# Optimization experiments

Hardware: AMD Instinct MI355X
Metric: run time of the kernel (lower is better)

Reference implementation:

```python
import jax, jax.numpy as jnp
import numpy as np

EMBED = 1024
HEADS = 16
HEAD_DIM = EMBED // HEADS

def setup_inputs() -> dict:
    key = jax.random.key(0)
    k1, k2, k3, k4, k5 = jax.random.split(key, 5)
    scale = 1.0 / np.sqrt(EMBED)
    return {
        "x": jax.random.normal(k1, (4, 2048, EMBED), dtype=jnp.float32),
        "qkv_w": jax.random.uniform(k2, (3 * EMBED, EMBED), minval=-scale, maxval=scale, dtype=jnp.float32),
        "qkv_b": jax.random.uniform(k3, (3 * EMBED,), minval=-scale, maxval=scale, dtype=jnp.float32),
        "out_w": jax.random.uniform(k4, (EMBED, EMBED), minval=-scale, maxval=scale, dtype=jnp.float32),
        "out_b": jax.random.uniform(k5, (EMBED,), minval=-scale, maxval=scale, dtype=jnp.float32),
    }

def reference(x, qkv_w, qkv_b, out_w, out_b):
    b, n, _ = x.shape
    # torch Linear: x @ W.T + b
    qkv = (jnp.einsum('bne,fe->bnf', x, qkv_w) + qkv_b).reshape(b, n, 3, HEADS, HEAD_DIM)
    q, k, v = qkv[:, :, 0], qkv[:, :, 1], qkv[:, :, 2]
    scores = jnp.einsum('bnhd,bmhd->bhnm', q, k) / jnp.sqrt(jnp.float32(HEAD_DIM))
    attn = jax.nn.softmax(scores, axis=-1)  # dropout p=0.0 -> identity
    out = jnp.einsum('bhnm,bmhd->bnhd', attn, v).reshape(b, n, EMBED)
    return jnp.einsum('bne,fe->bnf', out, out_w) + out_b
```

## Files before the change

kernel.cpp:

```cpp
#include <hip/hip_runtime.h>
#include <hip/hip_bf16.h>

typedef __bf16 bf16;
typedef __attribute__((ext_vector_type(8))) __bf16 bf16x8;
typedef __attribute__((ext_vector_type(4))) __bf16 bf16x4;
typedef __attribute__((ext_vector_type(4))) float f32x4;

#define EMBED 1024
#define HEADS 16
#define HD 64
#define NB 4
#define SEQ 2048
#define TOK (NB * SEQ)
#define F3 (3 * EMBED)

#define QSCALE 0.18033688011112042f
#define CEXP 16.0f

__device__ __forceinline__ float exp2_hw(float x) {
  float r;
  asm("v_exp_f32 %0, %1" : "=v"(r) : "v"(x));
  return r;
}

__device__ __forceinline__ void gload_lds16(const void* g, void* l) {
  __builtin_amdgcn_global_load_lds(
      (const __attribute__((address_space(1))) unsigned int*)(unsigned long long)g,
      (__attribute__((address_space(3))) unsigned int*)(unsigned int)(unsigned long long)l,
      16, 0, 0);
}

__global__ void cvt_bf16_kernel(const float* __restrict__ in, bf16* __restrict__ out, int n4) {
  int i = blockIdx.x * blockDim.x + threadIdx.x;
  if (i < n4) {
    float4 v = ((const float4*)in)[i];
    bf16x4 o;
    o[0] = (bf16)v.x; o[1] = (bf16)v.y; o[2] = (bf16)v.z; o[3] = (bf16)v.w;
    ((bf16x4*)out)[i] = o;
  }
}

template <int MODE, typename OUT_T>
__global__ __launch_bounds__(256) void gemm_bt(const bf16* __restrict__ A,
                                               const bf16* __restrict__ Bw,
                                               const float* __restrict__ bias,
                                               OUT_T* __restrict__ C,
                                               bf16* __restrict__ VT,
                                               int K, int Ncols) {
  __shared__ __align__(16) bf16 As[2][128 * 32];
  __shared__ __align__(16) bf16 Bs[2][128 * 32];

  const int tid = threadIdx.x;
  const int lane = tid & 63;
  const int w = tid >> 6;
  const int wr = w >> 1, wc = w & 1;
  const int lr = lane & 15, lg = lane >> 4;

  const int r0 = tid >> 2;
  const int csw = ((tid & 3) ^ ((tid >> 3) & 3)) * 8;
  const bf16* Ag = A + (size_t)blockIdx.x * 128 * K + (size_t)r0 * K + csw;
  const bf16* Bg = Bw + (size_t)blockIdx.y * 128 * K + (size_t)r0 * K + csw;

  f32x4 acc[4][4] = {};
  const int co = (lg ^ ((lr >> 1) & 3)) * 8;
  const int ntiles = K >> 5;

#define GSTAGE(buf)                                      \
  do {                                                   \
    gload_lds16(Ag, &As[buf][tid * 8]);                  \
    gload_lds16(Ag + 64 * K, &As[buf][(tid + 256) * 8]); \
    gload_lds16(Bg, &Bs[buf][tid * 8]);                  \
    gload_lds16(Bg + 64 * K, &Bs[buf][(tid + 256) * 8]); \
    Ag += 32; Bg += 32;                                  \
  } while (0)

  GSTAGE(0);
  __syncthreads();

  for (int t = 0; t < ntiles; ++t) {
    const int cur = t & 1;
    if (t + 1 < ntiles) GSTAGE(cur ^ 1);

    bf16x8 af[4], bfr[4];
#pragma unroll
    for (int mi = 0; mi < 4; ++mi)
      af[mi] = *(const bf16x8*)&As[cur][(wr * 64 + mi * 16 + lr) * 32 + co];
#pragma unroll
    for (int ni = 0; ni < 4; ++ni)
      bfr[ni] = *(const bf16x8*)&Bs[cur][(wc * 64 + ni * 16 + lr) * 32 + co];

#pragma unroll
    for (int mi = 0; mi < 4; ++mi)
#pragma unroll
      for (int ni = 0; ni < 4; ++ni)
        acc[mi][ni] = __builtin_amdgcn_mfma_f32_16x16x32_bf16(af[mi], bfr[ni], acc[mi][ni], 0, 0, 0);

    __syncthreads();
  }
#undef GSTAGE

  const int rowb = blockIdx.x * 128 + wr * 64;
  const int colb = blockIdx.y * 128 + wc * 64;

  if (MODE == 1 && blockIdx.y >= 16) {
#pragma unroll
    for (int ni = 0; ni < 4; ++ni) {
      int col = colb + ni * 16 + lr;
      int fc = col - 2 * EMBED;
      int hh = fc >> 6, d = fc & 63;
      float bv = bias[col];
#pragma unroll
      for (int mi = 0; mi < 4; ++mi) {
        int row = rowb + mi * 16 + lg * 4;
        int bb = row >> 11, nn = row & 2047;
        bf16x4 pk;
#pragma unroll
        for (int j = 0; j < 4; ++j) pk[j] = (bf16)(acc[mi][ni][j] + bv);
        *(bf16x4*)&VT[((size_t)((bb * HEADS + hh) * HD + d)) * SEQ + nn] = pk;
      }
    }
  } else {
    const float scale = (MODE == 1 && blockIdx.y < 8) ? QSCALE : 1.0f;
#pragma unroll
    for (int ni = 0; ni < 4; ++ni) {
      int col = colb + ni * 16 + lr;
      float bv = bias[col];
#pragma unroll
      for (int mi = 0; mi < 4; ++mi) {
#pragma unroll
        for (int j = 0; j < 4; ++j) {
          int row = rowb + mi * 16 + lg * 4 + j;
          C[(size_t)row * Ncols + col] = (OUT_T)((acc[mi][ni][j] + bv) * scale);
        }
      }
    }
  }
}

__global__ __launch_bounds__(256) void attn_fwd(const bf16* __restrict__ QK,
                                                const bf16* __restrict__ VT,
                                                bf16* __restrict__ O) {
  __shared__ __align__(16) bf16 Kb[2][64 * 64];
  __shared__ __align__(16) bf16 Vb[2][64 * 64];
  __shared__ __align__(16) bf16 Pl[4][32 * 76];

  const int qb = blockIdx.x, h = blockIdx.y, b = blockIdx.z;
  const int tid = threadIdx.x, lane = tid & 63, w = tid >> 6;
  const int lr = lane & 15, lg = lane >> 4;

  bf16x8 qf[2][2];
#pragma unroll
  for (int mi = 0; mi < 2; ++mi) {
    const bf16* qp = QK + (size_t)(b * SEQ + qb * 128 + w * 32 + mi * 16 + lr) * 2048 + h * HD + lg * 8;
    qf[mi][0] = *(const bf16x8*)qp;
    qf[mi][1] = *(const bf16x8*)(qp + 32);
  }

  const int rk = tid >> 3;
  const int cc = ((tid & 7) ^ (rk & 7)) * 8;
  const bf16* kp = QK + (size_t)(b * SEQ + rk) * 2048 + EMBED + h * HD + cc;
  const bf16* vp = VT + ((size_t)((b * HEADS + h) * HD + rk)) * SEQ + cc;

  f32x4 o[2][4] = {};
  f32x4 lp[2] = {};
  const f32x4 cinit = {-CEXP, -CEXP, -CEXP, -CEXP};
  const int swk = lr & 7;

#define ASTAGE(buf)                                       \
  do {                                                    \
    gload_lds16(kp, &Kb[buf][tid * 8]);                   \
    gload_lds16(kp + 32 * 2048, &Kb[buf][(tid + 256) * 8]); \
    gload_lds16(vp, &Vb[buf][tid * 8]);                   \
    gload_lds16(vp + 32 * SEQ, &Vb[buf][(tid + 256) * 8]); \
    kp += (size_t)64 * 2048; vp += 64;                    \
  } while (0)

  ASTAGE(0);
  __syncthreads();

  for (int t = 0; t < SEQ / 64; ++t) {
    const bf16* Kc = Kb[t & 1];
    const bf16* Vc = Vb[t & 1];
    if (t + 1 < SEQ / 64) ASTAGE((t & 1) ^ 1);

    f32x4 s[2][4];
    __builtin_amdgcn_s_setprio(1);
#pragma unroll
    for (int nt = 0; nt < 4; ++nt) {
      const bf16* kr = &Kc[(nt * 16 + lr) * 64];
      bf16x8 kf0 = *(const bf16x8*)&kr[(lg ^ swk) * 8];
      bf16x8 kf1 = *(const bf16x8*)&kr[((4 + lg) ^ swk) * 8];
#pragma unroll
      for (int mi = 0; mi < 2; ++mi) {
        f32x4 z = __builtin_amdgcn_mfma_f32_16x16x32_bf16(qf[mi][0], kf0, cinit, 0, 0, 0);
        s[mi][nt] = __builtin_amdgcn_mfma_f32_16x16x32_bf16(qf[mi][1], kf1, z, 0, 0, 0);
      }
    }
    __builtin_amdgcn_s_setprio(0);

#pragma unroll
    for (int mi = 0; mi < 2; ++mi) {
#pragma unroll
      for (int nt = 0; nt < 4; ++nt) {
        f32x4 p;
#pragma unroll
        for (int j = 0; j < 4; ++j) p[j] = exp2_hw(s[mi][nt][j]);
        lp[mi] += p;
#pragma unroll
        for (int j = 0; j < 4; ++j)
          Pl[w][(mi * 16 + lg * 4 + j) * 76 + nt * 16 + lr] = (bf16)p[j];
      }
    }
    asm volatile("s_waitcnt lgkmcnt(0)" ::: "memory");

    bf16x8 pfm[2][2];
#pragma unroll
    for (int mi = 0; mi < 2; ++mi)
#pragma unroll
      for (int ks = 0; ks < 2; ++ks)
        pfm[mi][ks] = *(const bf16x8*)&Pl[w][(mi * 16 + lr) * 76 + ks * 32 + lg * 8];
    __builtin_amdgcn_s_setprio(1);
#pragma unroll
    for (int dt = 0; dt < 4; ++dt) {
      const bf16* vr = &Vc[(dt * 16 + lr) * 64];
      bf16x8 vf0 = *(const bf16x8*)&vr[(lg ^ swk) * 8];
      bf16x8 vf1 = *(const bf16x8*)&vr[((4 + lg) ^ swk) * 8];
#pragma unroll
      for (int mi = 0; mi < 2; ++mi) {
        o[mi][dt] = __builtin_amdgcn_mfma_f32_16x16x32_bf16(pfm[mi][0], vf0, o[mi][dt], 0, 0, 0);
        o[mi][dt] = __builtin_amdgcn_mfma_f32_16x16x32_bf16(pfm[mi][1], vf1, o[mi][dt], 0, 0, 0);
      }
    }
    __builtin_amdgcn_s_setprio(0);

    __syncthreads();
  }
#undef ASTAGE

#pragma unroll
  for (int mi = 0; mi < 2; ++mi) {
#pragma unroll
    for (int j = 0; j < 4; ++j) {
      float r = lp[mi][j];
#pragma unroll
      for (int off = 1; off < 16; off <<= 1) r += __shfl_xor(r, off, 64);
      float rl = 1.0f / r;
      int trow = b * SEQ + qb * 128 + w * 32 + mi * 16 + lg * 4 + j;
#pragma unroll
      for (int dt = 0; dt < 4; ++dt)
        O[(size_t)trow * EMBED + h * HD + dt * 16 + lr] = (bf16)(o[mi][dt][j] * rl);
    }
  }
}

extern "C" void kernel_launch(void* const* d_in, const int* in_sizes, int n_in,
                              void* d_out, int out_size, void* d_ws, size_t ws_size,
                              hipStream_t stream) {
  const float* x     = (const float*)d_in[0];
  const float* qkv_w = (const float*)d_in[1];
  const float* qkv_b = (const float*)d_in[2];
  const float* out_w = (const float*)d_in[3];
  const float* out_b = (const float*)d_in[4];
  float* out = (float*)d_out;

  char* ws = (char*)d_ws;
  bf16* xb    = (bf16*)(ws);
  bf16* wqb   = (bf16*)(ws + 16777216);
  bf16* wob   = (bf16*)(ws + 23068672);
  bf16* qk    = (bf16*)(ws + 25165824);
  bf16* vT    = (bf16*)(ws + 58720256);
  bf16* attno = (bf16*)(ws + 75497472);

  cvt_bf16_kernel<<<(TOK * EMBED / 4 + 255) / 256, 256, 0, stream>>>(x, xb, TOK * EMBED / 4);
  cvt_bf16_kernel<<<(F3 * EMBED / 4 + 255) / 256, 256, 0, stream>>>(qkv_w, wqb, F3 * EMBED / 4);
  cvt_bf16_kernel<<<(EMBED * EMBED / 4 + 255) / 256, 256, 0, stream>>>(out_w, wob, EMBED * EMBED / 4);

  gemm_bt<1, bf16><<<dim3(TOK / 128, F3 / 128), 256, 0, stream>>>(xb, wqb, qkv_b, qk, vT, EMBED, 2048);

  attn_fwd<<<dim3(SEQ / 128, HEADS, NB), 256, 0, stream>>>(qk, vT, attno);

  gemm_bt<0, float><<<dim3(TOK / 128, EMBED / 128), 256, 0, stream>>>(attno, wob, out_b, out, nullptr, EMBED, EMBED);
}
```

Baseline: 302.2 us.

## Switch attention to 32x32 MFMA with register-resident P via permlane swaps

Rewrites the attention inner loop to use 32x32x16 bf16 MFMAs. QK^T is computed transposed (K as the A operand) so the exponentiated scores can be repacked into the PV A-operand in registers with cvt_pk_bf16 and permlane32_swap, removing the LDS round trip for P. Row sums reduce with a single cross-half shuffle. Launch bounds now request 4 blocks per CU, which may constrain registers.

```diff
diff --git a/kernel.cpp b/kernel.cpp
--- a/kernel.cpp
+++ b/kernel.cpp
@@ -5,6 +5,7 @@
 typedef __attribute__((ext_vector_type(8))) __bf16 bf16x8;
 typedef __attribute__((ext_vector_type(4))) __bf16 bf16x4;
 typedef __attribute__((ext_vector_type(4))) float f32x4;
+typedef __attribute__((ext_vector_type(16))) float f32x16;
 
 #define EMBED 1024
 #define HEADS 16
@@ -20,6 +21,12 @@
 __device__ __forceinline__ float exp2_hw(float x) {
   float r;
   asm("v_exp_f32 %0, %1" : "=v"(r) : "v"(x));
+  return r;
+}
+
+__device__ __forceinline__ unsigned int cvtpk_bf16(float lo, float hi) {
+  unsigned int r;
+  asm("v_cvt_pk_bf16_f32 %0, %1, %2" : "=v"(r) : "v"(lo), "v"(hi));
   return r;
 }
 
@@ -137,23 +144,23 @@
   }
 }
 
-__global__ __launch_bounds__(256) void attn_fwd(const bf16* __restrict__ QK,
-                                                const bf16* __restrict__ VT,
-                                                bf16* __restrict__ O) {
+__global__ __launch_bounds__(256, 4) void attn_fwd(const bf16* __restrict__ QK,
+                                                   const bf16* __restrict__ VT,
+                                                   bf16* __restrict__ O) {
   __shared__ __align__(16) bf16 Kb[2][64 * 64];
   __shared__ __align__(16) bf16 Vb[2][64 * 64];
-  __shared__ __align__(16) bf16 Pl[4][32 * 76];
+  __shared__ float Lrow[4][32];
 
   const int qb = blockIdx.x, h = blockIdx.y, b = blockIdx.z;
   const int tid = threadIdx.x, lane = tid & 63, w = tid >> 6;
-  const int lr = lane & 15, lg = lane >> 4;
-
-  bf16x8 qf[2][2];
-#pragma unroll
-  for (int mi = 0; mi < 2; ++mi) {
-    const bf16* qp = QK + (size_t)(b * SEQ + qb * 128 + w * 32 + mi * 16 + lr) * 2048 + h * HD + lg * 8;
-    qf[mi][0] = *(const bf16x8*)qp;
-    qf[mi][1] = *(const bf16x8*)(qp + 32);
+  const int lq = lane & 31, hi = lane >> 5;
+  const int sw = lq & 7;
+
+  bf16x8 qf[4];
+  {
+    const bf16* qp = QK + (size_t)(b * SEQ + qb * 128 + w * 32 + lq) * 2048 + h * HD + hi * 8;
+#pragma unroll
+    for (int c = 0; c < 4; ++c) qf[c] = *(const bf16x8*)(qp + c * 16);
   }
 
   const int rk = tid >> 3;
@@ -161,18 +168,19 @@
   const bf16* kp = QK + (size_t)(b * SEQ + rk) * 2048 + EMBED + h * HD + cc;
   const bf16* vp = VT + ((size_t)((b * HEADS + h) * HD + rk)) * SEQ + cc;
 
-  f32x4 o[2][4] = {};
-  f32x4 lp[2] = {};
-  const f32x4 cinit = {-CEXP, -CEXP, -CEXP, -CEXP};
-  const int swk = lr & 7;
-
-#define ASTAGE(buf)                                       \
-  do {                                                    \
-    gload_lds16(kp, &Kb[buf][tid * 8]);                   \
+  f32x16 oacc[2] = {};
+  float lp = 0.f;
+  f32x16 cinit;
+#pragma unroll
+  for (int r = 0; r < 16; ++r) cinit[r] = -CEXP;
+
+#define ASTAGE(buf)                                         \
+  do {                                                      \
+    gload_lds16(kp, &Kb[buf][tid * 8]);                     \
     gload_lds16(kp + 32 * 2048, &Kb[buf][(tid + 256) * 8]); \
-    gload_lds16(vp, &Vb[buf][tid * 8]);                   \
-    gload_lds16(vp + 32 * SEQ, &Vb[buf][(tid + 256) * 8]); \
-    kp += (size_t)64 * 2048; vp += 64;                    \
+    gload_lds16(vp, &Vb[buf][tid * 8]);                     \
+    gload_lds16(vp + 32 * SEQ, &Vb[buf][(tid + 256) * 8]);  \
+    kp += (size_t)64 * 2048; vp += 64;                      \
   } while (0)
 
   ASTAGE(0);
@@ -183,73 +191,66 @@
     const bf16* Vc = Vb[t & 1];
     if (t + 1 < SEQ / 64) ASTAGE((t & 1) ^ 1);
 
-    f32x4 s[2][4];
+    f32x16 s0 = cinit, s1 = cinit;
     __builtin_amdgcn_s_setprio(1);
 #pragma unroll
-    for (int nt = 0; nt < 4; ++nt) {
-      const bf16* kr = &Kc[(nt * 16 + lr) * 64];
-      bf16x8 kf0 = *(const bf16x8*)&kr[(lg ^ swk) * 8];
-      bf16x8 kf1 = *(const bf16x8*)&kr[((4 + lg) ^ swk) * 8];
-#pragma unroll
-      for (int mi = 0; mi < 2; ++mi) {
-        f32x4 z = __builtin_amdgcn_mfma_f32_16x16x32_bf16(qf[mi][0], kf0, cinit, 0, 0, 0);
-        s[mi][nt] = __builtin_amdgcn_mfma_f32_16x16x32_bf16(qf[mi][1], kf1, z, 0, 0, 0);
+    for (int c = 0; c < 4; ++c) {
+      const int cg = ((c * 2 + hi) ^ sw) * 8;
+      bf16x8 kf0 = *(const bf16x8*)&Kc[lq * 64 + cg];
+      bf16x8 kf1 = *(const bf16x8*)&Kc[(32 + lq) * 64 + cg];
+      s0 = __builtin_amdgcn_mfma_f32_32x32x16_bf16(kf0, qf[c], s0, 0, 0, 0);
+      s1 = __builtin_amdgcn_mfma_f32_32x32x16_bf16(kf1, qf[c], s1, 0, 0, 0);
+    }
+    __builtin_amdgcn_s_setprio(0);
+
+    bf16x8 pa[4];
+#pragma unroll
+    for (int g = 0; g < 2; ++g) {
+      const f32x16& sv = g ? s1 : s0;
+      float pv[16];
+#pragma unroll
+      for (int r = 0; r < 16; ++r) { pv[r] = exp2_hw(sv[r]); lp += pv[r]; }
+#pragma unroll
+      for (int cidx = 0; cidx < 2; ++cidx) {
+        const int pb = cidx * 8;
+        unsigned int x0 = cvtpk_bf16(pv[pb + 0], pv[pb + 1]);
+        unsigned int y0 = cvtpk_bf16(pv[pb + 4], pv[pb + 5]);
+        unsigned int x1 = cvtpk_bf16(pv[pb + 2], pv[pb + 3]);
+        unsigned int y1 = cvtpk_bf16(pv[pb + 6], pv[pb + 7]);
+        auto r0 = __builtin_amdgcn_permlane32_swap(x0, y0, false, false);
+        auto r1 = __builtin_amdgcn_permlane32_swap(x1, y1, false, false);
+        union { unsigned int u[4]; bf16x8 v; } fr;
+        fr.u[0] = r0[0]; fr.u[1] = r1[0]; fr.u[2] = r0[1]; fr.u[3] = r1[1];
+        pa[g * 2 + cidx] = fr.v;
       }
     }
+
+    __builtin_amdgcn_s_setprio(1);
+#pragma unroll
+    for (int k4 = 0; k4 < 4; ++k4) {
+      const int cg = ((k4 * 2 + hi) ^ sw) * 8;
+      bf16x8 vf0 = *(const bf16x8*)&Vc[lq * 64 + cg];
+      bf16x8 vf1 = *(const bf16x8*)&Vc[(32 + lq) * 64 + cg];
+      oacc[0] = __builtin_amdgcn_mfma_f32_32x32x16_bf16(pa[k4], vf0, oacc[0], 0, 0, 0);
+      oacc[1] = __builtin_amdgcn_mfma_f32_32x32x16_bf16(pa[k4], vf1, oacc[1], 0, 0, 0);
+    }
     __builtin_amdgcn_s_setprio(0);
 
-#pragma unroll
-    for (int mi = 0; mi < 2; ++mi) {
-#pragma unroll
-      for (int nt = 0; nt < 4; ++nt) {
-        f32x4 p;
-#pragma unroll
-        for (int j = 0; j < 4; ++j) p[j] = exp2_hw(s[mi][nt][j]);
-        lp[mi] += p;
-#pragma unroll
-        for (int j = 0; j < 4; ++j)
-          Pl[w][(mi * 16 + lg * 4 + j) * 76 + nt * 16 + lr] = (bf16)p[j];
-      }
-    }
-    asm volatile("s_waitcnt lgkmcnt(0)" ::: "memory");
-
-    bf16x8 pfm[2][2];
-#pragma unroll
-    for (int mi = 0; mi < 2; ++mi)
-#pragma unroll
-      for (int ks = 0; ks < 2; ++ks)
-        pfm[mi][ks] = *(const bf16x8*)&Pl[w][(mi * 16 + lr) * 76 + ks * 32 + lg * 8];
-    __builtin_amdgcn_s_setprio(1);
-#pragma unroll
-    for (int dt = 0; dt < 4; ++dt) {
-      const bf16* vr = &Vc[(dt * 16 + lr) * 64];
-      bf16x8 vf0 = *(const bf16x8*)&vr[(lg ^ swk) * 8];
-      bf16x8 vf1 = *(const bf16x8*)&vr[((4 + lg) ^ swk) * 8];
-#pragma unroll
-      for (int mi = 0; mi < 2; ++mi) {
-        o[mi][dt] = __builtin_amdgcn_mfma_f32_16x16x32_bf16(pfm[mi][0], vf0, o[mi][dt], 0, 0, 0);
-        o[mi][dt] = __builtin_amdgcn_mfma_f32_16x16x32_bf16(pfm[mi][1], vf1, o[mi][dt], 0, 0, 0);
-      }
-    }
-    __builtin_amdgcn_s_setprio(0);
-
     __syncthreads();
   }
 #undef ASTAGE
 
-#pragma unroll
-  for (int mi = 0; mi < 2; ++mi) {
-#pragma unroll
-    for (int j = 0; j < 4; ++j) {
-      float r = lp[mi][j];
-#pragma unroll
-      for (int off = 1; off < 16; off <<= 1) r += __shfl_xor(r, off, 64);
-      float rl = 1.0f / r;
-      int trow = b * SEQ + qb * 128 + w * 32 + mi * 16 + lg * 4 + j;
-#pragma unroll
-      for (int dt = 0; dt < 4; ++dt)
-        O[(size_t)trow * EMBED + h * HD + dt * 16 + lr] = (bf16)(o[mi][dt][j] * rl);
-    }
+  float lsum = lp + __shfl_xor(lp, 32, 64);
+  if (hi == 0) Lrow[w][lq] = 1.0f / lsum;
+  asm volatile("s_waitcnt lgkmcnt(0)" ::: "memory");
+
+  const size_t obase = (size_t)(b * SEQ + qb * 128 + w * 32) * EMBED + h * HD + lq;
+#pragma unroll
+  for (int r = 0; r < 16; ++r) {
+    const int qr = (r & 3) + 8 * (r >> 2) + 4 * hi;
+    const float rl = Lrow[w][qr];
+    O[obase + (size_t)qr * EMBED]      = (bf16)(oacc[0][r] * rl);
+    O[obase + (size_t)qr * EMBED + 32] = (bf16)(oacc[1][r] * rl);
   }
 }
 
```

After: 273.6 us. -9.5%, faster.
